# Kernel tuning notes

Measured on AMD Instinct MI355X. Metric: run time of the kernel, lower is better.

## Reference

```python
import jax, jax.numpy as jnp
import numpy as np
from jax import lax

H = 384
W = 384
N = H * W                 # flattened pixel count
N_LOC = N // 2            # unknown pixels with 3x3 matting-Laplacian stencils
KCM = 20                  # color-mixture KNN size
K_IU = 5                  # intra-unknown KNN size
NNZ_CM = N_LOC * KCM


def setup_inputs() -> dict:
    key = jax.random.key(0)
    ks = jax.random.split(key, 16)
    f32 = jnp.float32
    i32 = jnp.int32
    inp = {}
    inp["CM_weights"] = jax.random.uniform(ks[0], (N,), f32)
    inp["LOC_weights"] = jax.random.uniform(ks[1], (N,), f32)
    inp["IU_weights"] = jax.random.uniform(ks[2], (N,), f32)
    inp["KU_weights"] = jax.random.uniform(ks[3], (N,), f32)
    inp["lmbda"] = jnp.full((1,), 100.0, f32)
    inp["kToUconf"] = jax.random.uniform(ks[4], (N,), f32)
    inp["known"] = jax.random.uniform(ks[5], (N,), f32)
    inp["kToU"] = jax.random.uniform(ks[6], (N,), f32)
    inp["Wcm_data"] = jax.random.uniform(ks[7], (NNZ_CM,), f32)
    inp["LOC_flows"] = jax.random.uniform(ks[8], (9, 9, N_LOC), f32)
    inp["IU_flows"] = jax.random.uniform(ks[9], (N_LOC, K_IU), f32)
    inp["Wcm_row"] = jax.random.randint(ks[10], (NNZ_CM,), 0, N, dtype=i32)
    inp["Wcm_col"] = jax.random.randint(ks[11], (NNZ_CM,), 0, N, dtype=i32)
    # interior pixels so all 9 stencil neighbours are valid
    inp["LOC_inInd"] = jax.random.randint(ks[12], (N_LOC,), W + 1, N - W - 1, dtype=i32)
    inp["IU_inInd"] = jax.random.randint(ks[13], (N_LOC,), 0, N, dtype=i32)
    inp["IU_neighInd"] = jax.random.randint(ks[14], (N_LOC, K_IU), 0, N, dtype=i32)
    inp["width"] = W
    inp["cg_steps"] = 30
    return inp


def reference(CM_weights, LOC_weights, IU_weights, KU_weights, lmbda,
              kToUconf, known, kToU, Wcm_data, LOC_flows, IU_flows,
              Wcm_row, Wcm_col, LOC_inInd, IU_inInd, IU_neighInd,
              width, cg_steps):
    n = kToU.shape[0]
    seg = lambda v, i: jax.ops.segment_sum(v, i, num_segments=n)

    # --- color mixture: Wcm scaled by diag(CM_weights); L = diag(rowsum) - Wcm; Lcm = L^T L
    cm_vals = CM_weights[Wcm_row] * Wcm_data
    rs_cm = seg(cm_vals, Wcm_row)

    # --- matting Laplacian: 9x9 flows per unknown pixel over 3x3 stencil
    offs = jnp.array([-1 - width, -1, -1 + width, -width, 0, width,
                      1 - width, 1, 1 + width], dtype=LOC_inInd.dtype)
    neigh = LOC_inInd[:, None] + offs[None, :]                    # [n_loc, 9]
    fl = LOC_flows * LOC_weights[LOC_inInd][None, None, :]        # [9, 9, n_loc]
    nloc = neigh.shape[0]
    # entry (row=neigh[k,i], col=neigh[k,j]) has value fl[j, i, k]
    vals_m = jnp.transpose(fl, (2, 1, 0)).reshape(-1)
    rows_m = jnp.broadcast_to(neigh[:, :, None], (nloc, 9, 9)).reshape(-1)
    cols_m = jnp.broadcast_to(neigh[:, None, :], (nloc, 9, 9)).reshape(-1)
    rows_ms = jnp.concatenate([rows_m, cols_m])
    cols_ms = jnp.concatenate([cols_m, rows_m])
    vals_ms = 0.5 * jnp.concatenate([vals_m, vals_m])             # W = 0.5 (W + W^T)
    rs_m = seg(vals_ms, rows_ms)

    # --- intra-unknowns KNN affinities
    fiu = IU_flows * IU_weights[IU_inInd][:, None]                # [n_iu, K]
    rows_c0 = jnp.broadcast_to(IU_inInd[:, None], IU_neighInd.shape).reshape(-1)
    cols_c0 = IU_neighInd.reshape(-1)
    rows_cs = jnp.concatenate([rows_c0, cols_c0])
    cols_cs = jnp.concatenate([cols_c0, rows_c0])
    vals_cs = 0.5 * jnp.concatenate([fiu.reshape(-1), fiu.reshape(-1)])
    rs_c = seg(vals_cs, rows_cs)

    # --- diagonal data terms: KU + lmbda*known
    diag_ku = KU_weights * kToUconf + lmbda[0] * known
    b = diag_ku * kToU

    def matvec(v):
        # Lcm @ v = L^T (L v), keeping L in factored COO form
        Lv = rs_cm * v - seg(cm_vals * v[Wcm_col], Wcm_row)
        lcm = rs_cm * Lv - seg(cm_vals * Lv[Wcm_row], Wcm_col)
        lm = rs_m * v - seg(vals_ms * v[cols_ms], rows_ms)
        lc = rs_c * v - seg(vals_cs * v[cols_cs], rows_cs)
        return lcm + lm + lc + diag_ku * v

    def cg_step(carry, _):
        x, r, p, rs = carry
        Ap = matvec(p)
        alpha = rs / jnp.vdot(p, Ap)
        x = x + alpha * p
        r = r - alpha * Ap
        rs_new = jnp.vdot(r, r)
        p = r + (rs_new / rs) * p
        return (x, r, p, rs_new), None

    x0 = jnp.zeros_like(b)  # x0 = 0 as in MattingSolver
    (x, _, _, _), _ = lax.scan(cg_step, (x0, b, b, jnp.vdot(b, b)), None, length=cg_steps)
    return x
```

## Files before the change

kernel.cpp:

```cpp
#include <hip/hip_runtime.h>


#define TPB 256

__device__ __forceinline__ float blockReduce256(float v) {
  #pragma unroll
  for (int o = 32; o > 0; o >>= 1) v += __shfl_down(v, o, 64);
  __shared__ float s[4];
  int lane = threadIdx.x & 63, wv = threadIdx.x >> 6;
  if (lane == 0) s[wv] = v;
  __syncthreads();
  return (threadIdx.x == 0) ? (s[0] + s[1] + s[2] + s[3]) : 0.f;
}

__global__ void k_init0(const float* __restrict__ KUw, const float* __restrict__ kToUconf,
                        const float* __restrict__ lmbda, const float* __restrict__ known,
                        const float* __restrict__ kToU,
                        float* __restrict__ diag_ku, float* __restrict__ r,
                        float* __restrict__ p, float* __restrict__ x,
                        int* __restrict__ CNT, float* __restrict__ scal, int N)
{
  int i = blockIdx.x * TPB + threadIdx.x;
  if (i < 80) scal[i] = 0.f;
  if (i < 5 * N) CNT[i] = 0;
  float red = 0.f;
  if (i < N) {
    float dk = KUw[i] * kToUconf[i] + lmbda[0] * known[i];
    diag_ku[i] = dk;
    float b = dk * kToU[i];
    r[i] = b; p[i] = b; x[i] = 0.f;
    red = b * b;
  }
  float v = blockReduce256(red);
  if (threadIdx.x == 0) atomicAdd(&scal[0], v);
}

__global__ void k_prep(float* __restrict__ LOC_flows, const int* __restrict__ LOC_inInd,
                       const float* __restrict__ LOCw, int NLOC)
{
  int k = blockIdx.x * TPB + threadIdx.x;
  float Fl[81];
  #pragma unroll
  for (int m = 0; m < 81; ++m) Fl[m] = LOC_flows[(size_t)m * NLOC + k];
  float hw = 0.5f * LOCw[LOC_inInd[k]];
  int idx = 0;
  #pragma unroll
  for (int a = 0; a < 9; ++a)
    #pragma unroll
    for (int b = a + 1; b < 9; ++b) {
      LOC_flows[(size_t)idx * NLOC + k] = hw * (Fl[a * 9 + b] + Fl[b * 9 + a]);
      ++idx;
    }
}

__global__ void k_hist(const int* __restrict__ Wrow, const int* __restrict__ Wcol,
                       const int* __restrict__ LOC_inInd, const int* __restrict__ width_p,
                       const int* __restrict__ IU_inInd, const int* __restrict__ IU_neighInd,
                       int* __restrict__ CNT,
                       unsigned short* __restrict__ tr, unsigned short* __restrict__ tc,
                       unsigned short* __restrict__ tWm, unsigned short* __restrict__ tIU,
                       unsigned short* __restrict__ tB,
                       int NLOC, int N, int B0, int B1)
{
  int blk = blockIdx.x;
  if (blk < B0) {
    int e = blk * TPB + threadIdx.x;
    tr[e] = (unsigned short)atomicAdd(&CNT[Wrow[e]], 1);
    tc[e] = (unsigned short)atomicAdd(&CNT[N + Wcol[e]], 1);
  } else if (blk < B1) {
    int k = (blk - B0) * TPB + threadIdx.x;
    int wd = *width_p;
    int base = LOC_inInd[k];
    const int offs[9] = {-1 - wd, -1, -1 + wd, -wd, 0, wd, 1 - wd, 1, 1 + wd};
    #pragma unroll
    for (int a = 0; a < 9; ++a)
      tWm[a * NLOC + k] = (unsigned short)atomicAdd(&CNT[2 * N + base + offs[a]], 1);
  } else {
    int k = (blk - B1) * TPB + threadIdx.x;
    tIU[k] = (unsigned short)atomicAdd(&CNT[3 * N + IU_inInd[k]], 1);
    #pragma unroll
    for (int j = 0; j < 5; ++j)
      tB[j * NLOC + k] = (unsigned short)atomicAdd(&CNT[4 * N + IU_neighInd[k * 5 + j]], 1);
  }
}

__global__ void k_scan1(int* __restrict__ OFF, int* __restrict__ bsum, int tot)
{
  __shared__ int s[TPB];
  int gid = blockIdx.x * TPB + threadIdx.x;
  int v = (gid < tot) ? OFF[gid] : 0;
  s[threadIdx.x] = v;
  __syncthreads();
  #pragma unroll
  for (int o = 1; o < TPB; o <<= 1) {
    int t = (threadIdx.x >= o) ? s[threadIdx.x - o] : 0;
    __syncthreads();
    s[threadIdx.x] += t;
    __syncthreads();
  }
  if (gid < tot) OFF[gid] = s[threadIdx.x] - v;
  if (threadIdx.x == TPB - 1) bsum[blockIdx.x] = s[threadIdx.x];
}

__global__ void k_scan2(int* __restrict__ bsum, int nPerArr)
{
  __shared__ int s[1024];
  int base = blockIdx.x * nPerArr;
  int v = (threadIdx.x < nPerArr) ? bsum[base + threadIdx.x] : 0;
  s[threadIdx.x] = v;
  __syncthreads();
  for (int o = 1; o < 1024; o <<= 1) {
    int t = (threadIdx.x >= o) ? s[threadIdx.x - o] : 0;
    __syncthreads();
    s[threadIdx.x] += t;
    __syncthreads();
  }
  if (threadIdx.x < nPerArr) bsum[base + threadIdx.x] = s[threadIdx.x] - v;
}

__global__ void k_scan3(int* __restrict__ OFF, const int* __restrict__ bsum, int tot)
{
  int gid = blockIdx.x * TPB + threadIdx.x;
  if (gid < tot) OFF[gid] += bsum[blockIdx.x];
}

__global__ void k_fill(const float* __restrict__ CMw, const float* __restrict__ Wcm_data,
                       const int* __restrict__ Wrow, const int* __restrict__ Wcol,
                       const int* __restrict__ LOC_inInd, const int* __restrict__ width_p,
                       const int* __restrict__ IU_inInd, const int* __restrict__ IU_neighInd,
                       const int* __restrict__ OFF,
                       const unsigned short* __restrict__ tr, const unsigned short* __restrict__ tc,
                       const unsigned short* __restrict__ tWm, const unsigned short* __restrict__ tIU,
                       const unsigned short* __restrict__ tB,
                       int2* __restrict__ csrPk, int2* __restrict__ cscPk,
                       int* __restrict__ gIdxWm, int* __restrict__ kIU, int* __restrict__ gIdxB,
                       int NLOC, int N, int B0, int B1)
{
  int blk = blockIdx.x;
  if (blk < B0) {
    int e = blk * TPB + threadIdx.x;
    int row = Wrow[e], col = Wcol[e];
    int cv = __float_as_int(CMw[row] * Wcm_data[e]);
    csrPk[OFF[row] + tr[e]] = make_int2(col, cv);
    cscPk[OFF[N + col] + tc[e]] = make_int2(row, cv);
  } else if (blk < B1) {
    int k = (blk - B0) * TPB + threadIdx.x;
    int wd = *width_p;
    int base = LOC_inInd[k];
    const int offs[9] = {-1 - wd, -1, -1 + wd, -wd, 0, wd, 1 - wd, 1, 1 + wd};
    #pragma unroll
    for (int a = 0; a < 9; ++a)
      gIdxWm[OFF[2 * N + base + offs[a]] + tWm[a * NLOC + k]] = a * NLOC + k;
  } else {
    int k = (blk - B1) * TPB + threadIdx.x;
    kIU[OFF[3 * N + IU_inInd[k]] + tIU[k]] = k;
    #pragma unroll
    for (int j = 0; j < 5; ++j)
      gIdxB[OFF[4 * N + IU_neighInd[k * 5 + j]] + tB[j * NLOC + k]] = j * NLOC + k;
  }
}

__global__ void k_it1(const float* __restrict__ p,
                      const float* __restrict__ S2, const int* __restrict__ LOC_inInd,
                      const int* __restrict__ width_p,
                      const float* __restrict__ IU_flows, const int* __restrict__ IU_inInd,
                      const int* __restrict__ IU_neighInd, const float* __restrict__ IUw,
                      const float* __restrict__ diag_ku,
                      const int* __restrict__ OFF, const int2* __restrict__ csrPk,
                      float* __restrict__ u_all,
                      float* __restrict__ Lv, float* __restrict__ rs_cm,
                      float* __restrict__ pAp_t,
                      int NNZ, int NLOC, int N, int B0, int B1)
{
  int blk = blockIdx.x;
  float red = 0.f;
  if (blk < B0) {
    int k = blk * TPB + threadIdx.x;
    int wd = *width_p;
    int base = LOC_inInd[k];
    const int offs[9] = {-1 - wd, -1, -1 + wd, -wd, 0, wd, 1 - wd, 1, 1 + wd};
    float pv[9];
    #pragma unroll
    for (int a = 0; a < 9; ++a) pv[a] = p[base + offs[a]];
    float u[9] = {0.f, 0.f, 0.f, 0.f, 0.f, 0.f, 0.f, 0.f, 0.f};
    float qf = 0.f;
    int idx = 0;
    #pragma unroll
    for (int a = 0; a < 9; ++a)
      #pragma unroll
      for (int b = a + 1; b < 9; ++b) {
        float sv = S2[(size_t)idx * NLOC + k];
        ++idx;
        float d = pv[a] - pv[b];
        float t = sv * d;
        u[a] += t; u[b] -= t;
        qf += t * d;
      }
    #pragma unroll
    for (int a = 0; a < 9; ++a) u_all[a * NLOC + k] = u[a];
    red = qf;
  } else if (blk < B1) {
    int k = (blk - B0) * TPB + threadIdx.x;
    int r0 = IU_inInd[k];
    float hw = 0.5f * IUw[r0];
    float pr = p[r0];
    int c[5]; float w[5];
    #pragma unroll
    for (int j = 0; j < 5; ++j) {
      c[j] = IU_neighInd[k * 5 + j];
      w[j] = hw * IU_flows[k * 5 + j];
    }
    float pc[5];
    #pragma unroll
    for (int j = 0; j < 5; ++j) pc[j] = p[c[j]];
    float qf = 0.f, asum = 0.f;
    #pragma unroll
    for (int j = 0; j < 5; ++j) {
      float d = pr - pc[j];
      float uA = w[j] * d;
      u_all[(9 + j) * NLOC + k] = -uA;
      asum += uA;
      qf += uA * d;
    }
    u_all[14 * NLOC + k] = asum;
    red = qf;
  } else {
    int i = (blk - B1) * TPB + threadIdx.x;
    float pi = p[i];
    int s = OFF[i];
    int e = (i == N - 1) ? NNZ : OFF[i + 1];
    float acc = 0.f, rs = 0.f;
    int q = s;
    for (; q + 4 <= e; q += 4) {
      int2 e0 = csrPk[q];
      int2 e1 = csrPk[q + 1];
      int2 e2 = csrPk[q + 2];
      int2 e3 = csrPk[q + 3];
      float g0 = p[e0.x], g1 = p[e1.x], g2 = p[e2.x], g3 = p[e3.x];
      float c0 = __int_as_float(e0.y), c1 = __int_as_float(e1.y);
      float c2 = __int_as_float(e2.y), c3 = __int_as_float(e3.y);
      rs += (c0 + c1) + (c2 + c3);
      acc += c0 * (pi - g0) + c1 * (pi - g1) + c2 * (pi - g2) + c3 * (pi - g3);
    }
    for (; q < e; ++q) {
      int2 ed = csrPk[q];
      float cv = __int_as_float(ed.y);
      rs += cv;
      acc += cv * (pi - p[ed.x]);
    }
    Lv[i] = acc;
    rs_cm[i] = rs;
    red = diag_ku[i] * pi * pi + acc * acc;
  }
  float v = blockReduce256(red);
  if (threadIdx.x == 0) atomicAdd(pAp_t, v);
}

__global__ void k_it2(float* __restrict__ x, float* __restrict__ r,
                      const float* __restrict__ p, const float* __restrict__ Lv,
                      const float* __restrict__ rs_cm, const float* __restrict__ diag_ku,
                      const int* __restrict__ OFF,
                      const int2* __restrict__ cscPk,
                      const int* __restrict__ gIdxWm, const int* __restrict__ kIU,
                      const int* __restrict__ gIdxB, const float* __restrict__ u_all,
                      const float* __restrict__ rs_t, const float* __restrict__ pAp_t,
                      float* __restrict__ rs_t1,
                      int NNZ, int NLOC, int N)
{
  int i = blockIdx.x * TPB + threadIdx.x;
  float alpha = rs_t[0] / pAp_t[0];
  float tg = 0.f;
  {
    int s0 = OFF[2 * N + i];
    int e0 = (i == N - 1) ? 9 * NLOC : OFF[2 * N + i + 1];
    int q = s0;
    for (; q + 4 <= e0; q += 4) {
      int g0 = gIdxWm[q], g1 = gIdxWm[q + 1], g2 = gIdxWm[q + 2], g3 = gIdxWm[q + 3];
      float u0 = u_all[g0], u1 = u_all[g1], u2 = u_all[g2], u3 = u_all[g3];
      tg += (u0 + u1) + (u2 + u3);
    }
    for (; q < e0; ++q) tg += u_all[gIdxWm[q]];
  }
  {
    int s0 = OFF[3 * N + i];
    int e0 = (i == N - 1) ? NLOC : OFF[3 * N + i + 1];
    for (int q = s0; q < e0; ++q) tg += u_all[14 * NLOC + kIU[q]];
  }
  {
    int s0 = OFF[4 * N + i];
    int e0 = (i == N - 1) ? 5 * NLOC : OFF[4 * N + i + 1];
    int q = s0;
    for (; q + 4 <= e0; q += 4) {
      int g0 = gIdxB[q], g1 = gIdxB[q + 1], g2 = gIdxB[q + 2], g3 = gIdxB[q + 3];
      float u0 = u_all[9 * NLOC + g0], u1 = u_all[9 * NLOC + g1];
      float u2 = u_all[9 * NLOC + g2], u3 = u_all[9 * NLOC + g3];
      tg += (u0 + u1) + (u2 + u3);
    }
    for (; q < e0; ++q) tg += u_all[9 * NLOC + gIdxB[q]];
  }
  float sc = 0.f;
  {
    int s0 = OFF[N + i];
    int e0 = (i == N - 1) ? NNZ : OFF[N + i + 1];
    int q = s0;
    for (; q + 4 <= e0; q += 4) {
      int2 e0v = cscPk[q];
      int2 e1v = cscPk[q + 1];
      int2 e2v = cscPk[q + 2];
      int2 e3v = cscPk[q + 3];
      float l0 = Lv[e0v.x], l1 = Lv[e1v.x], l2 = Lv[e2v.x], l3 = Lv[e3v.x];
      sc += __int_as_float(e0v.y) * l0 + __int_as_float(e1v.y) * l1
          + __int_as_float(e2v.y) * l2 + __int_as_float(e3v.y) * l3;
    }
    for (; q < e0; ++q) {
      int2 ed = cscPk[q];
      sc += __int_as_float(ed.y) * Lv[ed.x];
    }
  }
  float pi = p[i];
  float Ap = diag_ku[i] * pi + rs_cm[i] * Lv[i] - sc + tg;
  x[i] += alpha * pi;
  float rn = r[i] - alpha * Ap;
  r[i] = rn;
  float v = blockReduce256(rn * rn);
  if (threadIdx.x == 0) atomicAdd(rs_t1, v);
}

__global__ void k_it3(float* __restrict__ p, const float* __restrict__ r,
                      const float* __restrict__ rs_new, const float* __restrict__ rs_old, int N)
{
  int i = blockIdx.x * TPB + threadIdx.x;
  float beta = rs_new[0] / rs_old[0];
  p[i] = r[i] + beta * p[i];
}

extern "C" void kernel_launch(void* const* d_in, const int* in_sizes, int n_in,
                              void* d_out, int out_size, void* d_ws, size_t ws_size,
                              hipStream_t stream)
{
  const float* CMw       = (const float*)d_in[0];
  const float* LOCw      = (const float*)d_in[1];
  const float* IUw       = (const float*)d_in[2];
  const float* KUw       = (const float*)d_in[3];
  const float* lmbda     = (const float*)d_in[4];
  const float* kToUconf  = (const float*)d_in[5];
  const float* known     = (const float*)d_in[6];
  const float* kToU      = (const float*)d_in[7];
  const float* Wcm_data  = (const float*)d_in[8];
  float*       LOC_flows = (float*)d_in[9];
  const float* IU_flows  = (const float*)d_in[10];
  const int*   Wrow      = (const int*)d_in[11];
  const int*   Wcol      = (const int*)d_in[12];
  const int*   LOC_inInd = (const int*)d_in[13];
  const int*   IU_inInd  = (const int*)d_in[14];
  const int*   IU_neighInd = (const int*)d_in[15];
  const int*   width_p   = (const int*)d_in[16];
  const int CG_STEPS = 30;

  const int N    = in_sizes[0];
  const int NNZ  = in_sizes[8];
  const int NLOC = in_sizes[13];

  float* x       = (float*)d_out;
  float* r       = (float*)d_ws;
  float* p       = r + N;
  float* Lv      = p + N;
  float* rs_cm   = Lv + N;
  float* diag_ku = rs_cm + N;
  int2*  csrPk   = (int2*)(diag_ku + N);
  int2*  cscPk   = csrPk + (size_t)NNZ;
  int*   gIdxWm  = (int*)(cscPk + (size_t)NNZ);
  int*   kIU     = gIdxWm + (size_t)9 * NLOC;
  int*   gIdxB   = kIU + (size_t)NLOC;
  int*   OFF     = gIdxB + (size_t)5 * NLOC;
  unsigned short* tr  = (unsigned short*)(OFF + (size_t)5 * N);
  unsigned short* tc  = tr + (size_t)NNZ;
  unsigned short* tWm = tc + (size_t)NNZ;
  unsigned short* tIU = tWm + (size_t)9 * NLOC;
  unsigned short* tB  = tIU + (size_t)NLOC;
  float* u_all   = (float*)tr;
  int*   bsum    = (int*)(tB + (size_t)5 * NLOC);
  float* scal    = (float*)(bsum + 5 * (N / TPB));

  const int Bn = N / TPB;
  const int Bz = NNZ / TPB;
  const int Bl = NLOC / TPB;
  const int Z5 = 5 * Bn;

  k_init0<<<Z5, TPB, 0, stream>>>(KUw, kToUconf, lmbda, known, kToU,
                                  diag_ku, r, p, x, OFF, scal, N);
  k_prep<<<Bl, TPB, 0, stream>>>(LOC_flows, LOC_inInd, LOCw, NLOC);
  k_hist<<<Bz + 2 * Bl, TPB, 0, stream>>>(Wrow, Wcol, LOC_inInd, width_p,
                                          IU_inInd, IU_neighInd, OFF,
                                          tr, tc, tWm, tIU, tB,
                                          NLOC, N, Bz, Bz + Bl);
  k_scan1<<<Z5, TPB, 0, stream>>>(OFF, bsum, 5 * N);
  k_scan2<<<5, 1024, 0, stream>>>(bsum, Bn);
  k_scan3<<<Z5, TPB, 0, stream>>>(OFF, bsum, 5 * N);
  k_fill<<<Bz + 2 * Bl, TPB, 0, stream>>>(CMw, Wcm_data, Wrow, Wcol,
                                          LOC_inInd, width_p, IU_inInd, IU_neighInd,
                                          OFF, tr, tc, tWm, tIU, tB,
                                          csrPk, cscPk, gIdxWm, kIU, gIdxB,
                                          NLOC, N, Bz, Bz + Bl);

  for (int t = 0; t < CG_STEPS; ++t) {
    k_it1<<<2 * Bl + Bn, TPB, 0, stream>>>(
        p, LOC_flows, LOC_inInd, width_p,
        IU_flows, IU_inInd, IU_neighInd, IUw,
        diag_ku, OFF, csrPk, u_all, Lv, rs_cm, scal + 40 + t,
        NNZ, NLOC, N, Bl, 2 * Bl);
    k_it2<<<Bn, TPB, 0, stream>>>(
        x, r, p, Lv, rs_cm, diag_ku, OFF, cscPk, gIdxWm, kIU, gIdxB, u_all,
        scal + t, scal + 40 + t, scal + t + 1, NNZ, NLOC, N);
    if (t + 1 < CG_STEPS)
      k_it3<<<Bn, TPB, 0, stream>>>(p, r, scal + t + 1, scal + t, N);
  }
}
```

Baseline: 1.957 ms.

## Merge matting and intra-unknown scatter lists into one CSR; unroll gathers by 8

Folds the three per-pixel transpose lists (matting stencil, IU centre, IU neighbour) into one combined CSR over 15*NLOC u_all entries, so k_it2 walks a single segment per pixel instead of three. This cuts the histogram and scan setup from five count arrays to three and removes two offset loads and loop overheads per pixel in each CG iteration. The CSR gather loops in k_it1 and k_it2 also get an 8-wide unrolled stage, which puts more loads in flight at the cost of more registers. The fill order within a row now depends on atomics across all sources together, so the summation order changes slightly.

```diff
diff --git a/kernel.cpp b/kernel.cpp
--- a/kernel.cpp
+++ b/kernel.cpp
@@ -22,7 +22,7 @@
 {
   int i = blockIdx.x * TPB + threadIdx.x;
   if (i < 80) scal[i] = 0.f;
-  if (i < 5 * N) CNT[i] = 0;
+  if (i < 3 * N) CNT[i] = 0;
   float red = 0.f;
   if (i < N) {
     float dk = KUw[i] * kToUconf[i] + lmbda[0] * known[i];
@@ -58,8 +58,7 @@
                        const int* __restrict__ IU_inInd, const int* __restrict__ IU_neighInd,
                        int* __restrict__ CNT,
                        unsigned short* __restrict__ tr, unsigned short* __restrict__ tc,
-                       unsigned short* __restrict__ tWm, unsigned short* __restrict__ tIU,
-                       unsigned short* __restrict__ tB,
+                       unsigned short* __restrict__ tU,
                        int NLOC, int N, int B0, int B1)
 {
   int blk = blockIdx.x;
@@ -74,13 +73,14 @@
     const int offs[9] = {-1 - wd, -1, -1 + wd, -wd, 0, wd, 1 - wd, 1, 1 + wd};
     #pragma unroll
     for (int a = 0; a < 9; ++a)
-      tWm[a * NLOC + k] = (unsigned short)atomicAdd(&CNT[2 * N + base + offs[a]], 1);
+      tU[a * NLOC + k] = (unsigned short)atomicAdd(&CNT[2 * N + base + offs[a]], 1);
   } else {
     int k = (blk - B1) * TPB + threadIdx.x;
-    tIU[k] = (unsigned short)atomicAdd(&CNT[3 * N + IU_inInd[k]], 1);
+    tU[14 * NLOC + k] = (unsigned short)atomicAdd(&CNT[2 * N + IU_inInd[k]], 1);
     #pragma unroll
     for (int j = 0; j < 5; ++j)
-      tB[j * NLOC + k] = (unsigned short)atomicAdd(&CNT[4 * N + IU_neighInd[k * 5 + j]], 1);
+      tU[(9 + j) * NLOC + k] =
+          (unsigned short)atomicAdd(&CNT[2 * N + IU_neighInd[k * 5 + j]], 1);
   }
 }
 
@@ -130,10 +130,9 @@
                        const int* __restrict__ IU_inInd, const int* __restrict__ IU_neighInd,
                        const int* __restrict__ OFF,
                        const unsigned short* __restrict__ tr, const unsigned short* __restrict__ tc,
-                       const unsigned short* __restrict__ tWm, const unsigned short* __restrict__ tIU,
-                       const unsigned short* __restrict__ tB,
+                       const unsigned short* __restrict__ tU,
                        int2* __restrict__ csrPk, int2* __restrict__ cscPk,
-                       int* __restrict__ gIdxWm, int* __restrict__ kIU, int* __restrict__ gIdxB,
+                       int* __restrict__ gU,
                        int NLOC, int N, int B0, int B1)
 {
   int blk = blockIdx.x;
@@ -150,13 +149,14 @@
     const int offs[9] = {-1 - wd, -1, -1 + wd, -wd, 0, wd, 1 - wd, 1, 1 + wd};
     #pragma unroll
     for (int a = 0; a < 9; ++a)
-      gIdxWm[OFF[2 * N + base + offs[a]] + tWm[a * NLOC + k]] = a * NLOC + k;
+      gU[OFF[2 * N + base + offs[a]] + tU[a * NLOC + k]] = a * NLOC + k;
   } else {
     int k = (blk - B1) * TPB + threadIdx.x;
-    kIU[OFF[3 * N + IU_inInd[k]] + tIU[k]] = k;
+    gU[OFF[2 * N + IU_inInd[k]] + tU[14 * NLOC + k]] = 14 * NLOC + k;
     #pragma unroll
     for (int j = 0; j < 5; ++j)
-      gIdxB[OFF[4 * N + IU_neighInd[k * 5 + j]] + tB[j * NLOC + k]] = j * NLOC + k;
+      gU[OFF[2 * N + IU_neighInd[k * 5 + j]] + tU[(9 + j) * NLOC + k]] =
+          (9 + j) * NLOC + k;
   }
 }
 
@@ -231,16 +231,33 @@
     int e = (i == N - 1) ? NNZ : OFF[i + 1];
     float acc = 0.f, rs = 0.f;
     int q = s;
+    for (; q + 8 <= e; q += 8) {
+      int2 ed[8];
+      #pragma unroll
+      for (int m = 0; m < 8; ++m) ed[m] = csrPk[q + m];
+      float g[8];
+      #pragma unroll
+      for (int m = 0; m < 8; ++m) g[m] = p[ed[m].x];
+      #pragma unroll
+      for (int m = 0; m < 8; ++m) {
+        float cv = __int_as_float(ed[m].y);
+        rs += cv;
+        acc += cv * (pi - g[m]);
+      }
+    }
     for (; q + 4 <= e; q += 4) {
-      int2 e0 = csrPk[q];
-      int2 e1 = csrPk[q + 1];
-      int2 e2 = csrPk[q + 2];
-      int2 e3 = csrPk[q + 3];
-      float g0 = p[e0.x], g1 = p[e1.x], g2 = p[e2.x], g3 = p[e3.x];
-      float c0 = __int_as_float(e0.y), c1 = __int_as_float(e1.y);
-      float c2 = __int_as_float(e2.y), c3 = __int_as_float(e3.y);
-      rs += (c0 + c1) + (c2 + c3);
-      acc += c0 * (pi - g0) + c1 * (pi - g1) + c2 * (pi - g2) + c3 * (pi - g3);
+      int2 ed[4];
+      #pragma unroll
+      for (int m = 0; m < 4; ++m) ed[m] = csrPk[q + m];
+      float g[4];
+      #pragma unroll
+      for (int m = 0; m < 4; ++m) g[m] = p[ed[m].x];
+      #pragma unroll
+      for (int m = 0; m < 4; ++m) {
+        float cv = __int_as_float(ed[m].y);
+        rs += cv;
+        acc += cv * (pi - g[m]);
+      }
     }
     for (; q < e; ++q) {
       int2 ed = csrPk[q];
@@ -261,8 +278,7 @@
                       const float* __restrict__ rs_cm, const float* __restrict__ diag_ku,
                       const int* __restrict__ OFF,
                       const int2* __restrict__ cscPk,
-                      const int* __restrict__ gIdxWm, const int* __restrict__ kIU,
-                      const int* __restrict__ gIdxB, const float* __restrict__ u_all,
+                      const int* __restrict__ gU, const float* __restrict__ u_all,
                       const float* __restrict__ rs_t, const float* __restrict__ pAp_t,
                       float* __restrict__ rs_t1,
                       int NNZ, int NLOC, int N)
@@ -272,45 +288,54 @@
   float tg = 0.f;
   {
     int s0 = OFF[2 * N + i];
-    int e0 = (i == N - 1) ? 9 * NLOC : OFF[2 * N + i + 1];
+    int e0 = (i == N - 1) ? 15 * NLOC : OFF[2 * N + i + 1];
     int q = s0;
+    for (; q + 8 <= e0; q += 8) {
+      int g[8];
+      #pragma unroll
+      for (int m = 0; m < 8; ++m) g[m] = gU[q + m];
+      float u[8];
+      #pragma unroll
+      for (int m = 0; m < 8; ++m) u[m] = u_all[g[m]];
+      #pragma unroll
+      for (int m = 0; m < 8; ++m) tg += u[m];
+    }
     for (; q + 4 <= e0; q += 4) {
-      int g0 = gIdxWm[q], g1 = gIdxWm[q + 1], g2 = gIdxWm[q + 2], g3 = gIdxWm[q + 3];
-      float u0 = u_all[g0], u1 = u_all[g1], u2 = u_all[g2], u3 = u_all[g3];
-      tg += (u0 + u1) + (u2 + u3);
-    }
-    for (; q < e0; ++q) tg += u_all[gIdxWm[q]];
-  }
-  {
-    int s0 = OFF[3 * N + i];
-    int e0 = (i == N - 1) ? NLOC : OFF[3 * N + i + 1];
-    for (int q = s0; q < e0; ++q) tg += u_all[14 * NLOC + kIU[q]];
-  }
-  {
-    int s0 = OFF[4 * N + i];
-    int e0 = (i == N - 1) ? 5 * NLOC : OFF[4 * N + i + 1];
-    int q = s0;
-    for (; q + 4 <= e0; q += 4) {
-      int g0 = gIdxB[q], g1 = gIdxB[q + 1], g2 = gIdxB[q + 2], g3 = gIdxB[q + 3];
-      float u0 = u_all[9 * NLOC + g0], u1 = u_all[9 * NLOC + g1];
-      float u2 = u_all[9 * NLOC + g2], u3 = u_all[9 * NLOC + g3];
-      tg += (u0 + u1) + (u2 + u3);
-    }
-    for (; q < e0; ++q) tg += u_all[9 * NLOC + gIdxB[q]];
+      int g[4];
+      #pragma unroll
+      for (int m = 0; m < 4; ++m) g[m] = gU[q + m];
+      float u[4];
+      #pragma unroll
+      for (int m = 0; m < 4; ++m) u[m] = u_all[g[m]];
+      #pragma unroll
+      for (int m = 0; m < 4; ++m) tg += u[m];
+    }
+    for (; q < e0; ++q) tg += u_all[gU[q]];
   }
   float sc = 0.f;
   {
     int s0 = OFF[N + i];
     int e0 = (i == N - 1) ? NNZ : OFF[N + i + 1];
     int q = s0;
+    for (; q + 8 <= e0; q += 8) {
+      int2 ed[8];
+      #pragma unroll
+      for (int m = 0; m < 8; ++m) ed[m] = cscPk[q + m];
+      float l[8];
+      #pragma unroll
+      for (int m = 0; m < 8; ++m) l[m] = Lv[ed[m].x];
+      #pragma unroll
+      for (int m = 0; m < 8; ++m) sc += __int_as_float(ed[m].y) * l[m];
+    }
     for (; q + 4 <= e0; q += 4) {
-      int2 e0v = cscPk[q];
-      int2 e1v = cscPk[q + 1];
-      int2 e2v = cscPk[q + 2];
-      int2 e3v = cscPk[q + 3];
-      float l0 = Lv[e0v.x], l1 = Lv[e1v.x], l2 = Lv[e2v.x], l3 = Lv[e3v.x];
-      sc += __int_as_float(e0v.y) * l0 + __int_as_float(e1v.y) * l1
-          + __int_as_float(e2v.y) * l2 + __int_as_float(e3v.y) * l3;
+      int2 ed[4];
+      #pragma unroll
+      for (int m = 0; m < 4; ++m) ed[m] = cscPk[q + m];
+      float l[4];
+      #pragma unroll
+      for (int m = 0; m < 4; ++m) l[m] = Lv[ed[m].x];
+      #pragma unroll
+      for (int m = 0; m < 4; ++m) sc += __int_as_float(ed[m].y) * l[m];
     }
     for (; q < e0; ++q) {
       int2 ed = cscPk[q];
@@ -369,38 +394,33 @@
   float* diag_ku = rs_cm + N;
   int2*  csrPk   = (int2*)(diag_ku + N);
   int2*  cscPk   = csrPk + (size_t)NNZ;
-  int*   gIdxWm  = (int*)(cscPk + (size_t)NNZ);
-  int*   kIU     = gIdxWm + (size_t)9 * NLOC;
-  int*   gIdxB   = kIU + (size_t)NLOC;
-  int*   OFF     = gIdxB + (size_t)5 * NLOC;
-  unsigned short* tr  = (unsigned short*)(OFF + (size_t)5 * N);
-  unsigned short* tc  = tr + (size_t)NNZ;
-  unsigned short* tWm = tc + (size_t)NNZ;
-  unsigned short* tIU = tWm + (size_t)9 * NLOC;
-  unsigned short* tB  = tIU + (size_t)NLOC;
+  int*   gU      = (int*)(cscPk + (size_t)NNZ);
+  int*   OFF     = gU + (size_t)15 * NLOC;
+  unsigned short* tr = (unsigned short*)(OFF + (size_t)3 * N);
+  unsigned short* tc = tr + (size_t)NNZ;
+  unsigned short* tU = tc + (size_t)NNZ;
   float* u_all   = (float*)tr;
-  int*   bsum    = (int*)(tB + (size_t)5 * NLOC);
-  float* scal    = (float*)(bsum + 5 * (N / TPB));
+  int*   bsum    = (int*)(tU + (size_t)15 * NLOC);
+  float* scal    = (float*)(bsum + 3 * (N / TPB));
 
   const int Bn = N / TPB;
   const int Bz = NNZ / TPB;
   const int Bl = NLOC / TPB;
-  const int Z5 = 5 * Bn;
-
-  k_init0<<<Z5, TPB, 0, stream>>>(KUw, kToUconf, lmbda, known, kToU,
+  const int Z3 = 3 * Bn;
+
+  k_init0<<<Z3, TPB, 0, stream>>>(KUw, kToUconf, lmbda, known, kToU,
                                   diag_ku, r, p, x, OFF, scal, N);
   k_prep<<<Bl, TPB, 0, stream>>>(LOC_flows, LOC_inInd, LOCw, NLOC);
   k_hist<<<Bz + 2 * Bl, TPB, 0, stream>>>(Wrow, Wcol, LOC_inInd, width_p,
                                           IU_inInd, IU_neighInd, OFF,
-                                          tr, tc, tWm, tIU, tB,
-                                          NLOC, N, Bz, Bz + Bl);
-  k_scan1<<<Z5, TPB, 0, stream>>>(OFF, bsum, 5 * N);
-  k_scan2<<<5, 1024, 0, stream>>>(bsum, Bn);
-  k_scan3<<<Z5, TPB, 0, stream>>>(OFF, bsum, 5 * N);
+                                          tr, tc, tU, NLOC, N, Bz, Bz + Bl);
+  k_scan1<<<Z3, TPB, 0, stream>>>(OFF, bsum, 3 * N);
+  k_scan2<<<3, 1024, 0, stream>>>(bsum, Bn);
+  k_scan3<<<Z3, TPB, 0, stream>>>(OFF, bsum, 3 * N);
   k_fill<<<Bz + 2 * Bl, TPB, 0, stream>>>(CMw, Wcm_data, Wrow, Wcol,
                                           LOC_inInd, width_p, IU_inInd, IU_neighInd,
-                                          OFF, tr, tc, tWm, tIU, tB,
-                                          csrPk, cscPk, gIdxWm, kIU, gIdxB,
+                                          OFF, tr, tc, tU,
+                                          csrPk, cscPk, gU,
                                           NLOC, N, Bz, Bz + Bl);
 
   for (int t = 0; t < CG_STEPS; ++t) {
@@ -410,7 +430,7 @@
         diag_ku, OFF, csrPk, u_all, Lv, rs_cm, scal + 40 + t,
         NNZ, NLOC, N, Bl, 2 * Bl);
     k_it2<<<Bn, TPB, 0, stream>>>(
-        x, r, p, Lv, rs_cm, diag_ku, OFF, cscPk, gIdxWm, kIU, gIdxB, u_all,
+        x, r, p, Lv, rs_cm, diag_ku, OFF, cscPk, gU, u_all,
         scal + t, scal + 40 + t, scal + t + 1, NNZ, NLOC, N);
     if (t + 1 < CG_STEPS)
       k_it3<<<Bn, TPB, 0, stream>>>(p, r, scal + t + 1, scal + t, N);
```

Result: faster. 1.871 ms, median of 2 (-4.4%).
